# Kernel tuning notes

Measured on AMD Instinct MI355X. Metric: run time of the kernel, lower is better.

## Reference

```python
import jax, jax.numpy as jnp
import numpy as np

ATTN_HEADS = 4
NEG = -1e9
LN_EPS = 1e-5


def _ln(x, s, b):
    m = x.mean(-1, keepdims=True)
    v = ((x - m) ** 2).mean(-1, keepdims=True)
    return (x - m) * jax.lax.rsqrt(v + LN_EPS) * s + b


def setup_inputs() -> dict:
    key = jax.random.key(0)
    ks = jax.random.split(key, 40)
    B, L, D, FF, NL = 512, 192, 256, 1024, 2
    V, U, I = 30000, 100000, 50000
    Lp, Ln, NF = 30, 300, 13
    Lu = jax.random.randint(ks[0], (B,), 1, L // 2)
    Li = jax.random.randint(ks[1], (B,), 1, L // 2)
    inp = {
        'attr': jax.random.randint(ks[2], (B, L), 0, V),
        'attr_inds': jax.random.randint(ks[3], (B, L), 0, 3),
        'attr_tf': jax.random.uniform(ks[4], (B, L), dtype=jnp.float32),
        'attr_feat': jax.random.normal(ks[5], (B, L, NF), dtype=jnp.float32),
        'attr_lens': Lu + Li,
        'attr_lens_user': Lu,
        'attr_lens_item': Li,
        'user_ids': jax.random.randint(ks[6], (B,), 0, U),
        'item_ids': jax.random.randint(ks[7], (B,), 0, I),
        'pos_targets': jax.random.randint(ks[8], (B, Lp), 0, V),
        'pos_lens': jax.random.randint(ks[9], (B,), 1, Lp + 1),
        'neg_targets': jax.random.randint(ks[10], (B, Ln), 0, V),
        'neg_lens': jax.random.randint(ks[11], (B,), 1, Ln + 1),
        # embedding tables (uniform(-0.1,0.1) per f_init_weight)
        'attr_emb': jax.random.uniform(ks[12], (V, D), minval=-0.1, maxval=0.1),
        'ind_emb': jax.random.uniform(ks[13], (3, D), minval=-0.1, maxval=0.1),
        'user_emb_table': jax.random.uniform(ks[14], (U, D), minval=-0.1, maxval=0.1),
        'item_emb_table': jax.random.uniform(ks[15], (I, D), minval=-0.1, maxval=0.1),
        'out_emb_user': jax.random.uniform(ks[16], (V, 2 * D), minval=-0.1, maxval=0.1),
        'out_emb_item': jax.random.uniform(ks[17], (V, 2 * D), minval=-0.1, maxval=0.1),
        # attr-weight head: Linear(13,1) + sigmoid
        'feat_w': jax.random.normal(ks[18], (NF,)) * 0.02,
        'feat_b': jnp.zeros(()),
        # transformer encoder params, stacked over NL layers
        'Wqkv': jax.random.normal(ks[19], (NL, 3 * D, D)) * 0.02,
        'bqkv': jnp.zeros((NL, 3 * D)),
        'Wo': jax.random.normal(ks[20], (NL, D, D)) * 0.02,
        'bo': jnp.zeros((NL, D)),
        'ln1_s': jnp.ones((NL, D)), 'ln1_b': jnp.zeros((NL, D)),
        'W1': jax.random.normal(ks[21], (NL, FF, D)) * 0.02,
        'b1': jnp.zeros((NL, FF)),
        'W2': jax.random.normal(ks[22], (NL, D, FF)) * 0.02,
        'b2': jnp.zeros((NL, D)),
        'ln2_s': jnp.ones((NL, D)), 'ln2_b': jnp.zeros((NL, D)),
    }
    return inp


def reference(attr, attr_inds, attr_tf, attr_feat, attr_lens, attr_lens_user,
              attr_lens_item, user_ids, item_ids, pos_targets, pos_lens,
              neg_targets, neg_lens, attr_emb, ind_emb, user_emb_table,
              item_emb_table, out_emb_user, out_emb_item, feat_w, feat_b,
              Wqkv, bqkv, Wo, bo, ln1_s, ln1_b, W1, b1, W2, b2, ln2_s, ln2_b):
    B, L = attr.shape
    D = attr_emb.shape[1]
    NL = Wqkv.shape[0]
    Dh = D // ATTN_HEADS
    pos = jnp.arange(L)
    valid = pos[None, :] < attr_lens[:, None]  # [B,L] True = valid key

    x = attr_emb[attr] + ind_emb[attr_inds]  # [B,L,D]
    for l in range(NL):  # post-LN TransformerEncoderLayer, relu, no dropout
        qkv = x @ Wqkv[l].T + bqkv[l]
        q, k, v = jnp.split(qkv, 3, axis=-1)
        q = q.reshape(B, L, ATTN_HEADS, Dh).transpose(0, 2, 1, 3)
        k = k.reshape(B, L, ATTN_HEADS, Dh).transpose(0, 2, 1, 3)
        v = v.reshape(B, L, ATTN_HEADS, Dh).transpose(0, 2, 1, 3)
        scores = jnp.einsum('bhqd,bhkd->bhqk', q, k) / np.sqrt(Dh).astype(x.dtype)
        scores = jnp.where(valid[:, None, None, :], scores, NEG)
        a = jax.nn.softmax(scores, axis=-1)
        ctx = jnp.einsum('bhqk,bhkd->bhqd', a, v).transpose(0, 2, 1, 3).reshape(B, L, D)
        x = _ln(x + ctx @ Wo[l].T + bo[l], ln1_s[l], ln1_b[l])
        ff = jax.nn.relu(x @ W1[l].T + b1[l]) @ W2[l].T + b2[l]
        x = _ln(x + ff, ln2_s[l], ln2_b[l])

    # ragged weighted segment average over user span [0,Lu) and item span [Lu,Lu+Li)
    w_user = jax.nn.sigmoid(attr_feat @ feat_w + feat_b)  # [B,L]
    wted = x * attr_tf[..., None]
    umask = pos[None, :] < attr_lens_user[:, None]
    imask = (~umask) & (pos[None, :] < (attr_lens_user + attr_lens_item)[:, None])
    user_x = (wted * w_user[..., None] * umask[..., None]).sum(1) / attr_lens_user[:, None].astype(x.dtype)
    item_x = (wted * (1.0 - w_user)[..., None] * imask[..., None]).sum(1) / attr_lens_item[:, None].astype(x.dtype)

    user_out = jnp.concatenate([user_x, user_emb_table[user_ids]], axis=-1)  # [B,2D]
    item_out = jnp.concatenate([item_x, item_emb_table[item_ids]], axis=-1)

    def logit(t):
        return (jnp.einsum('bkd,bd->bk', out_emb_user[t], user_out)
                + jnp.einsum('bkd,bd->bk', out_emb_item[t], item_out))

    pos_logits = logit(pos_targets)
    neg_logits = logit(neg_targets)
    pmask = jnp.arange(pos_targets.shape[1])[None, :] < pos_lens[:, None]
    nmask = jnp.arange(neg_targets.shape[1])[None, :] < neg_lens[:, None]
    logits = jnp.concatenate([pos_logits, neg_logits], axis=-1)
    mask = jnp.concatenate([pmask, nmask], axis=-1)
    new_targets = jnp.concatenate([jnp.ones_like(pos_targets), jnp.zeros_like(neg_targets)], axis=1) * mask
    return logits, mask, new_targets
```

## Files before the change

kernel.cpp:

```cpp
#include <hip/hip_runtime.h>
#include <hip/hip_bf16.h>
#include <cstdint>
#include <cstddef>

#define B_ 512
#define L_ 192
#define D_ 256
#define H_ 4
#define DH_ 64
#define FF_ 1024
#define NL_ 2
#define LP_ 30
#define LNEG_ 300
#define NF_ 13
#define M_ (B_*L_)
#define NT_ 330
#define V_ 30000

typedef __attribute__((ext_vector_type(8))) short bf16x8;
typedef __attribute__((ext_vector_type(4))) float f32x4;

__device__ __forceinline__ ushort f2b(float f) {
  union { float f; uint32_t u; } v; v.f = f;
  uint32_t u = v.u;
  return (ushort)((u + 0x7FFFu + ((u >> 16) & 1u)) >> 16);
}
__device__ __forceinline__ float b2f(ushort u) {
  union { uint32_t u; float f; } v; v.u = (uint32_t)u << 16; return v.f;
}
__device__ __forceinline__ void stage16(const ushort* src, char* dst) {
  __builtin_amdgcn_global_load_lds((const __attribute__((address_space(1))) unsigned int*)src,
                                   (__attribute__((address_space(3))) unsigned int*)dst, 16, 0, 0);
}

__global__ __launch_bounds__(512) void k_prefix(
    const int* __restrict__ lens, int* __restrict__ off,
    int* __restrict__ ccnt, int* __restrict__ ccntp, int Bc, int nchunks)
{
  const int t = threadIdx.x;
  int s = 0;
  for (int i = 0; i < t; ++i) s += lens[i];
  off[t] = s;
  if (t == 511) off[512] = s + lens[511];
  if (t < nchunks) {
    int s2 = 0;
    const int c0 = t * Bc;
    for (int i = 0; i < Bc; ++i) s2 += lens[c0 + i];
    ccnt[t]  = s2;
    ccntp[t] = (s2 + 127) & ~127;
  }
}

__global__ __launch_bounds__(256) void k_f2b(const float* __restrict__ in, ushort* __restrict__ out) {
  const int i = (blockIdx.x*256 + threadIdx.x)*8;
  float4 a = *(const float4*)(in+i);
  float4 b = *(const float4*)(in+i+4);
  ushort4 o1; o1.x=f2b(a.x); o1.y=f2b(a.y); o1.z=f2b(a.z); o1.w=f2b(a.w);
  ushort4 o2; o2.x=f2b(b.x); o2.y=f2b(b.y); o2.z=f2b(b.z); o2.w=f2b(b.w);
  *(ushort4*)(out+i)   = o1;
  *(ushort4*)(out+i+4) = o2;
}

__global__ __launch_bounds__(256) void k_f2b4(
    const float* __restrict__ wq, const float* __restrict__ wo,
    const float* __restrict__ w1, const float* __restrict__ w2,
    ushort* __restrict__ oq, ushort* __restrict__ oo,
    ushort* __restrict__ o1, ushort* __restrict__ o2)
{
  int bb = blockIdx.x;
  const float* in; ushort* out; int base;
  if (bb < 192)      { in = wq; out = oq; base = bb; }
  else if (bb < 256) { in = wo; out = oo; base = bb - 192; }
  else if (bb < 512) { in = w1; out = o1; base = bb - 256; }
  else               { in = w2; out = o2; base = bb - 512; }
  const int i = base*2048 + threadIdx.x*8;
  float4 a = *(const float4*)(in+i);
  float4 b = *(const float4*)(in+i+4);
  ushort4 q1; q1.x=f2b(a.x); q1.y=f2b(a.y); q1.z=f2b(a.z); q1.w=f2b(a.w);
  ushort4 q2; q2.x=f2b(b.x); q2.y=f2b(b.y); q2.z=f2b(b.z); q2.w=f2b(b.w);
  *(ushort4*)(out+i)   = q1;
  *(ushort4*)(out+i+4) = q2;
}

__global__ __launch_bounds__(256) void k_embed(
    const int* __restrict__ attr, const int* __restrict__ inds,
    const int* __restrict__ lens, const int* __restrict__ off,
    const float* __restrict__ attr_emb, const float* __restrict__ ind_emb,
    ushort* __restrict__ xb)
{
  int idx = blockIdx.x*256 + threadIdx.x;
  int token = idx >> 6;
  int c = (idx & 63) * 4;
  int b = token / L_;
  int l = token - b*L_;
  if (l >= lens[b]) return;
  size_t crow = (size_t)off[b] + l;
  int a = attr[token];
  int id = inds[token];
  const float4 e  = *(const float4*)(attr_emb + (size_t)a*D_ + c);
  const float4 ie = *(const float4*)(ind_emb  + (size_t)id*D_ + c);
  ushort4 ob; ob.x=f2b(e.x+ie.x); ob.y=f2b(e.y+ie.y); ob.z=f2b(e.z+ie.z); ob.w=f2b(e.w+ie.w);
  *(ushort4*)(xb + crow*D_ + c) = ob;
}

template<int OUT_BF16, int RELU>
__global__ __launch_bounds__(256) void k_gemm_mfma(
    const ushort* __restrict__ A, const int* __restrict__ aoffp,
    const int* __restrict__ cntp,
    const ushort* __restrict__ W, const float* __restrict__ bias,
    void* __restrict__ Cv, int N, int K)
{
  if ((int)blockIdx.y * 128 >= *cntp) return;
  __shared__ alignas(16) ushort As[8192];
  __shared__ alignas(16) ushort Bs[8192];
  const int abase = *aoffp;
  const int tid = threadIdx.x;
  const int w = tid >> 6, l = tid & 63;
  const int g = l >> 4, c16 = l & 15;
  const int m0 = blockIdx.y*128, n0 = blockIdx.x*128;
  const int wr = w >> 1, wc = w & 1;
  const int swzr = (c16 & 7) << 4;

  f32x4 acc[4][4];
  #pragma unroll
  for (int i=0;i<4;++i)
    #pragma unroll
    for (int j=0;j<4;++j) acc[i][j] = (f32x4){0.f,0.f,0.f,0.f};

  for (int k0=0; k0<K; k0+=64) {
    #pragma unroll
    for (int i=0;i<4;++i) {
      const int li  = i*4096 + tid*16;
      const int row = li >> 7;
      const int col = ((li & 127) ^ ((row & 7) << 4)) >> 1;
      stage16(A + (size_t)(abase+m0+row)*K + k0 + col, (char*)(As) + i*4096 + w*1024);
      stage16(W + (size_t)(n0+row)*K + k0 + col,       (char*)(Bs) + i*4096 + w*1024);
    }
    __syncthreads();
    #pragma unroll
    for (int ks=0; ks<2; ++ks) {
      const int cb = ((g*16 + ks*64) ^ swzr) >> 1;
      bf16x8 af[4], bfr[4];
      #pragma unroll
      for (int i2=0;i2<4;++i2) {
        af[i2]  = *(const bf16x8*)(As + (size_t)(wr*64 + i2*16 + c16)*64 + cb);
        bfr[i2] = *(const bf16x8*)(Bs + (size_t)(wc*64 + i2*16 + c16)*64 + cb);
      }
      #pragma unroll
      for (int mi=0;mi<4;++mi)
        #pragma unroll
        for (int ni=0;ni<4;++ni)
          acc[mi][ni] = __builtin_amdgcn_mfma_f32_16x16x32_bf16(bfr[ni], af[mi], acc[mi][ni], 0,0,0);
    }
    __syncthreads();
  }
  #pragma unroll
  for (int ni=0;ni<4;++ni) {
    const int nc = n0 + wc*64 + ni*16 + 4*g;
    const float4 bv = *(const float4*)(bias + nc);
    #pragma unroll
    for (int mi=0;mi<4;++mi) {
      float v0 = acc[mi][ni][0] + bv.x;
      float v1 = acc[mi][ni][1] + bv.y;
      float v2 = acc[mi][ni][2] + bv.z;
      float v3 = acc[mi][ni][3] + bv.w;
      if (RELU) { v0=fmaxf(v0,0.f); v1=fmaxf(v1,0.f); v2=fmaxf(v2,0.f); v3=fmaxf(v3,0.f); }
      const size_t idx = (size_t)(m0 + wr*64 + mi*16 + c16)*N + nc;
      if (OUT_BF16) {
        ushort4 o; o.x=f2b(v0); o.y=f2b(v1); o.z=f2b(v2); o.w=f2b(v3);
        *(ushort4*)((ushort*)Cv + idx) = o;
      } else {
        float4 o; o.x=v0; o.y=v1; o.z=v2; o.w=v3;
        *(float4*)((float*)Cv + idx) = o;
      }
    }
  }
}

__global__ __launch_bounds__(512) void k_gemm_ln(
    const ushort* __restrict__ A,
    const int* __restrict__ cntp, const int* __restrict__ cnt,
    const int* __restrict__ xoffp,
    const ushort* __restrict__ W,
    const float* __restrict__ bias,
    const float* __restrict__ lns, const float* __restrict__ lnb,
    ushort* __restrict__ xb, int K)
{
  const int m0 = blockIdx.x*128;
  if (m0 >= *cntp) return;
  __shared__ alignas(16) ushort As[8192];
  __shared__ alignas(16) ushort Bs[16384];
  __shared__ float red[4][2][128];
  const int tid = threadIdx.x;
  const int w = tid >> 6, l = tid & 63;
  const int g = l >> 4, c16 = l & 15;
  const int wr = w >> 2, wc = w & 3;
  const int swzr = (c16 & 7) << 4;

  f32x4 acc[4][4];
  #pragma unroll
  for (int i=0;i<4;++i)
    #pragma unroll
    for (int j=0;j<4;++j) acc[i][j] = (f32x4){0.f,0.f,0.f,0.f};

  for (int k0=0; k0<K; k0+=64) {
    #pragma unroll
    for (int i=0;i<2;++i) {
      const int li  = i*8192 + tid*16;
      const int row = li >> 7;
      const int col = ((li & 127) ^ ((row & 7) << 4)) >> 1;
      stage16(A + (size_t)(m0+row)*K + k0 + col, (char*)(As) + i*8192 + w*1024);
    }
    #pragma unroll
    for (int i=0;i<4;++i) {
      const int li  = i*8192 + tid*16;
      const int row = li >> 7;
      const int col = ((li & 127) ^ ((row & 7) << 4)) >> 1;
      stage16(W + (size_t)row*K + k0 + col, (char*)(Bs) + i*8192 + w*1024);
    }
    __syncthreads();
    #pragma unroll
    for (int ks=0; ks<2; ++ks) {
      const int cb = ((g*16 + ks*64) ^ swzr) >> 1;
      bf16x8 af[4], bfr[4];
      #pragma unroll
      for (int i2=0;i2<4;++i2) {
        af[i2]  = *(const bf16x8*)(As + (size_t)(wr*64 + i2*16 + c16)*64 + cb);
        bfr[i2] = *(const bf16x8*)(Bs + (size_t)(wc*64 + i2*16 + c16)*64 + cb);
      }
      #pragma unroll
      for (int mi=0;mi<4;++mi)
        #pragma unroll
        for (int ni=0;ni<4;++ni)
          acc[mi][ni] = __builtin_amdgcn_mfma_f32_16x16x32_bf16(bfr[ni], af[mi], acc[mi][ni], 0,0,0);
    }
    __syncthreads();
  }

  const int xbase = *xoffp + m0;
  float4 bv[4], sv[4], bb[4];
  #pragma unroll
  for (int ni=0;ni<4;++ni) {
    const int nc = wc*64 + ni*16 + 4*g;
    bv[ni] = *(const float4*)(bias + nc);
    sv[ni] = *(const float4*)(lns + nc);
    bb[ni] = *(const float4*)(lnb + nc);
  }
  float ps[4], pq[4];
  #pragma unroll
  for (int mi=0;mi<4;++mi) {
    ps[mi]=0.f; pq[mi]=0.f;
    const int lrow = wr*64 + mi*16 + c16;
    const ushort* xr = xb + (size_t)(xbase + lrow)*256;
    #pragma unroll
    for (int ni=0;ni<4;++ni) {
      const int nc = wc*64 + ni*16 + 4*g;
      ushort4 rx = *(const ushort4*)(xr + nc);
      float y0 = acc[mi][ni][0] + bv[ni].x + b2f(rx.x);
      float y1 = acc[mi][ni][1] + bv[ni].y + b2f(rx.y);
      float y2 = acc[mi][ni][2] + bv[ni].z + b2f(rx.z);
      float y3 = acc[mi][ni][3] + bv[ni].w + b2f(rx.w);
      acc[mi][ni][0]=y0; acc[mi][ni][1]=y1; acc[mi][ni][2]=y2; acc[mi][ni][3]=y3;
      ps[mi] += (y0+y1)+(y2+y3);
      pq[mi] += (y0*y0+y1*y1)+(y2*y2+y3*y3);
    }
  }
  #pragma unroll
  for (int mi=0;mi<4;++mi) {
    ps[mi] += __shfl_xor(ps[mi], 16, 64);
    pq[mi] += __shfl_xor(pq[mi], 16, 64);
    ps[mi] += __shfl_xor(ps[mi], 32, 64);
    pq[mi] += __shfl_xor(pq[mi], 32, 64);
  }
  if (g == 0) {
    #pragma unroll
    for (int mi=0;mi<4;++mi) {
      const int lrow = wr*64 + mi*16 + c16;
      red[wc][0][lrow] = ps[mi];
      red[wc][1][lrow] = pq[mi];
    }
  }
  __syncthreads();
  const int cexact = *cnt;
  #pragma unroll
  for (int mi=0;mi<4;++mi) {
    const int lrow = wr*64 + mi*16 + c16;
    float tsum = red[0][0][lrow] + red[1][0][lrow] + red[2][0][lrow] + red[3][0][lrow];
    float tsq  = red[0][1][lrow] + red[1][1][lrow] + red[2][1][lrow] + red[3][1][lrow];
    float mean = tsum * (1.f/256.f);
    float var  = tsq * (1.f/256.f) - mean*mean;
    float inv  = rsqrtf(var + 1e-5f);
    if (m0 + lrow < cexact) {
      ushort* xbr = xb + (size_t)(xbase + lrow)*256;
      #pragma unroll
      for (int ni=0;ni<4;++ni) {
        const int nc = wc*64 + ni*16 + 4*g;
        ushort4 o;
        o.x = f2b((acc[mi][ni][0]-mean)*inv*sv[ni].x + bb[ni].x);
        o.y = f2b((acc[mi][ni][1]-mean)*inv*sv[ni].y + bb[ni].y);
        o.z = f2b((acc[mi][ni][2]-mean)*inv*sv[ni].z + bb[ni].z);
        o.w = f2b((acc[mi][ni][3]-mean)*inv*sv[ni].w + bb[ni].w);
        *(ushort4*)(xbr + nc) = o;
      }
    }
  }
}

__global__ __launch_bounds__(512) void k_ffn(
    const int* __restrict__ cntp, const int* __restrict__ cnt,
    const int* __restrict__ xoffp,
    const ushort* __restrict__ W1, const float* __restrict__ b1,
    const ushort* __restrict__ W2, const float* __restrict__ b2,
    const float* __restrict__ lns, const float* __restrict__ lnb,
    ushort* __restrict__ xb)
{
  const int m0 = blockIdx.x*64;
  if (m0 >= *cntp) return;
  __shared__ alignas(16) char lds[98304];
  char* Xs = lds;
  char* Wb = lds + 32768;
  char* Hs = lds + 81920;
  float* red = (float*)(lds + 32768);
  const int tid = threadIdx.x;
  const int w = tid >> 6, l = tid & 63;
  const int g = l >> 4, c16 = l & 15;
  const int wr = w >> 2, wc = w & 3;
  const int swzr = (c16 & 7) << 4;
  const int xbase = *xoffp + m0;

  int tokl[2];
  #pragma unroll
  for (int mi=0;mi<2;++mi) tokl[mi] = wr*32 + mi*16 + c16;

  auto stage_chunk = [&](int s, int q, char* dst) {
    #pragma unroll
    for (int i=0;i<2;++i) {
      const int li = i*8192 + tid*16;
      const int row = li >> 7;
      const int colb = (li & 127) ^ ((row & 7) << 4);
      const ushort* src;
      if (q < 4) src = W1 + (size_t)(s*128+row)*256 + q*64 + (colb>>1);
      else {
        const int t2 = q - 4;
        src = W2 + (size_t)((t2>>1)*128+row)*1024 + s*128 + (t2&1)*64 + (colb>>1);
      }
      stage16(src, dst + i*8192 + w*1024);
    }
  };

  #pragma unroll
  for (int i=0;i<4;++i) {
    const int li = i*8192 + tid*16;
    const int row = li >> 9;
    const int colb = (li & 511) ^ ((row & 7) << 4);
    stage16(xb + (size_t)(xbase+row)*256 + (colb>>1), Xs + i*8192 + w*1024);
  }
  stage_chunk(0, 0, Wb);
  stage_chunk(0, 1, Wb + 16384);
  asm volatile("s_waitcnt vmcnt(2) lgkmcnt(0)" ::: "memory");
  __builtin_amdgcn_s_barrier();
  __builtin_amdgcn_sched_barrier(0);

  f32x4 tac[2][4];
  #pragma unroll
  for (int i=0;i<2;++i)
    #pragma unroll
    for (int j=0;j<4;++j) tac[i][j] = (f32x4){0.f,0.f,0.f,0.f};

  int cur = 0;
  for (int s=0; s<8; ++s) {
    f32x4 hac[2][2];
    #pragma unroll
    for (int i=0;i<2;++i)
      #pragma unroll
      for (int j=0;j<2;++j) hac[i][j] = (f32x4){0.f,0.f,0.f,0.f};

    #pragma unroll
    for (int q=0; q<8; ++q) {
      if (q < 6) {
        stage_chunk(s, q+2, Wb + ((cur+2)%3)*16384);
      } else if (s < 7) {
        stage_chunk(s+1, q-6, Wb + ((cur+2)%3)*16384);
      }
      char* curbuf = Wb + cur*16384;

      if (q < 4) {
        #pragma unroll
        for (int ks=0; ks<2; ++ks) {
          const int cbw = (ks*64 + g*16) ^ swzr;
          bf16x8 w1f[2], xf[2];
          #pragma unroll
          for (int ni=0;ni<2;++ni)
            w1f[ni] = *(const bf16x8*)(curbuf + (wc*32 + ni*16 + c16)*128 + cbw);
          #pragma unroll
          for (int mi=0;mi<2;++mi)
            xf[mi] = *(const bf16x8*)(Xs + tokl[mi]*512 + ((q*128 + ks*64 + g*16) ^ swzr));
          #pragma unroll
          for (int mi=0;mi<2;++mi)
            #pragma unroll
            for (int ni=0;ni<2;++ni)
              hac[mi][ni] = __builtin_amdgcn_mfma_f32_16x16x32_bf16(w1f[ni], xf[mi], hac[mi][ni], 0,0,0);
        }
        if (q == 3) {
          #pragma unroll
          for (int ni=0;ni<2;++ni) {
            const int ffc = wc*32 + ni*16 + 4*g;
            const float4 bb1 = *(const float4*)(b1 + s*128 + ffc);
            #pragma unroll
            for (int mi=0;mi<2;++mi) {
              ushort4 o;
              o.x = f2b(fmaxf(hac[mi][ni][0] + bb1.x, 0.f));
              o.y = f2b(fmaxf(hac[mi][ni][1] + bb1.y, 0.f));
              o.z = f2b(fmaxf(hac[mi][ni][2] + bb1.z, 0.f));
              o.w = f2b(fmaxf(hac[mi][ni][3] + bb1.w, 0.f));
              *(ushort4*)(Hs + tokl[mi]*256 + ((ffc*2) ^ swzr)) = o;
            }
          }
        }
      } else {
        const int dh = (q-4) >> 1, kc2 = (q-4) & 1;
        #pragma unroll
        for (int ks=0; ks<2; ++ks) {
          const int cbw = (ks*64 + g*16) ^ swzr;
          bf16x8 w2f[2], hf[2];
          #pragma unroll
          for (int ni=0;ni<2;++ni)
            w2f[ni] = *(const bf16x8*)(curbuf + (wc*32 + ni*16 + c16)*128 + cbw);
          #pragma unroll
          for (int mi=0;mi<2;++mi)
            hf[mi] = *(const bf16x8*)(Hs + tokl[mi]*256 + ((kc2*128 + ks*64 + g*16) ^ swzr));
          #pragma unroll
          for (int mi=0;mi<2;++mi)
            #pragma unroll
            for (int ni=0;ni<2;++ni)
              tac[mi][dh*2+ni] = __builtin_amdgcn_mfma_f32_16x16x32_bf16(w2f[ni], hf[mi], tac[mi][dh*2+ni], 0,0,0);
        }
      }

      if (q >= 6) {
        if (s == 7) { asm volatile("s_waitcnt vmcnt(0) lgkmcnt(0)" ::: "memory"); }
        else        { asm volatile("s_waitcnt vmcnt(2) lgkmcnt(0)" ::: "memory"); }
      } else {
        asm volatile("s_waitcnt vmcnt(2) lgkmcnt(0)" ::: "memory");
      }
      __builtin_amdgcn_s_barrier();
      __builtin_amdgcn_sched_barrier(0);
      cur = (cur + 1) % 3;
    }
  }

  float4 bv[4], sv[4], bb[4];
  #pragma unroll
  for (int n=0;n<4;++n) {
    const int nc = (n>>1)*128 + wc*32 + (n&1)*16 + 4*g;
    bv[n] = *(const float4*)(b2 + nc);
    sv[n] = *(const float4*)(lns + nc);
    bb[n] = *(const float4*)(lnb + nc);
  }
  float ps[2], pq[2];
  #pragma unroll
  for (int mi=0;mi<2;++mi) {
    ps[mi]=0.f; pq[mi]=0.f;
    const ushort* xr = xb + (size_t)(xbase + tokl[mi])*256;
    #pragma unroll
    for (int n=0;n<4;++n) {
      const int nc = (n>>1)*128 + wc*32 + (n&1)*16 + 4*g;
      ushort4 rx = *(const ushort4*)(xr + nc);
      float y0 = tac[mi][n][0] + bv[n].x + b2f(rx.x);
      float y1 = tac[mi][n][1] + bv[n].y + b2f(rx.y);
      float y2 = tac[mi][n][2] + bv[n].z + b2f(rx.z);
      float y3 = tac[mi][n][3] + bv[n].w + b2f(rx.w);
      tac[mi][n][0]=y0; tac[mi][n][1]=y1; tac[mi][n][2]=y2; tac[mi][n][3]=y3;
      ps[mi] += (y0+y1)+(y2+y3);
      pq[mi] += (y0*y0+y1*y1)+(y2*y2+y3*y3);
    }
  }
  #pragma unroll
  for (int mi=0;mi<2;++mi) {
    ps[mi] += __shfl_xor(ps[mi], 16, 64);
    pq[mi] += __shfl_xor(pq[mi], 16, 64);
    ps[mi] += __shfl_xor(ps[mi], 32, 64);
    pq[mi] += __shfl_xor(pq[mi], 32, 64);
  }
  if (g == 0) {
    #pragma unroll
    for (int mi=0;mi<2;++mi) {
      red[(wc*2+0)*64 + tokl[mi]] = ps[mi];
      red[(wc*2+1)*64 + tokl[mi]] = pq[mi];
    }
  }
  __syncthreads();
  const int cexact = *cnt;
  #pragma unroll
  for (int mi=0;mi<2;++mi) {
    const int lrow = tokl[mi];
    float tsum = red[0*64+lrow] + red[2*64+lrow] + red[4*64+lrow] + red[6*64+lrow];
    float tsq  = red[1*64+lrow] + red[3*64+lrow] + red[5*64+lrow] + red[7*64+lrow];
    float mean = tsum * (1.f/256.f);
    float var  = tsq * (1.f/256.f) - mean*mean;
    float inv  = rsqrtf(var + 1e-5f);
    if (m0 + lrow < cexact) {
      ushort* xbr = xb + (size_t)(xbase + lrow)*256;
      #pragma unroll
      for (int n=0;n<4;++n) {
        const int nc = (n>>1)*128 + wc*32 + (n&1)*16 + 4*g;
        ushort4 o;
        o.x = f2b((tac[mi][n][0]-mean)*inv*sv[n].x + bb[n].x);
        o.y = f2b((tac[mi][n][1]-mean)*inv*sv[n].y + bb[n].y);
        o.z = f2b((tac[mi][n][2]-mean)*inv*sv[n].z + bb[n].z);
        o.w = f2b((tac[mi][n][3]-mean)*inv*sv[n].w + bb[n].w);
        *(ushort4*)(xbr + nc) = o;
      }
    }
  }
}

__global__ __launch_bounds__(256) void k_attn_mfma(
    const ushort* __restrict__ qkv, ushort* __restrict__ ctx,
    const int* __restrict__ offc)
{
  __shared__ alignas(16) char lds[81920];
  char* Kb = lds;
  char* Vt = lds + 24576;
  const int tid = threadIdx.x;
  const int w = tid >> 6, l = tid & 63;
  const int g = l >> 4, c = l & 15;
  char* Pw = lds + 57344 + w*6144;
  const int bl = blockIdx.x >> 2, h = blockIdx.x & 3;
  const int rowbase = offc[bl] - offc[0];
  const int len = offc[bl+1] - offc[bl];
  const int nkt = (len + 15) >> 4;
  const int nkf = (len + 31) >> 5;
  const ushort* base = qkv + (size_t)rowbase*768;
  ushort* cbase = ctx + (size_t)rowbase*256;

  const int lenk8 = nkt*16*8;
  for (int idx = tid; idx < lenk8; idx += 256) {
    int row = idx >> 3, ch = idx & 7;
    uint4 v = *(const uint4*)(base + (size_t)row*768 + 256 + h*64 + ch*8);
    *(uint4*)(Kb + ((row*128 + ch*16) ^ ((row&7)<<4))) = v;
  }
  {
    const int lenv = nkf*32;
    int d0 = (tid & 15)*4;
    for (int key = tid >> 4; key < lenv; key += 16) {
      ushort4 v = *(const ushort4*)(base + (size_t)key*768 + 512 + h*64 + d0);
      ushort vv[4] = {v.x, v.y, v.z, v.w};
      #pragma unroll
      for (int j=0;j<4;++j) {
        int d = d0 + j;
        *(ushort*)(Vt + ((d*512 + key*2) ^ ((d&7)<<4))) = vv[j];
      }
    }
  }
  __syncthreads();

  for (int t = nkt; t < 2*nkf; ++t) {
    #pragma unroll
    for (int r=0;r<4;++r) {
      int q = 4*g + r;
      *(ushort*)(Pw + (((t>>1)*1024 + q*64 + ((t&1)*16 + c)*2) ^ (((q>>2)&3)<<4))) = 0;
    }
  }

  const int nst = (len + 15) >> 4;
  for (int s = w; s < nst; s += 4) {
    const ushort* qp = base + (size_t)(s*16 + c)*768 + h*64 + g*8;
    bf16x8 aq0 = *(const bf16x8*)qp;
    bf16x8 aq1 = *(const bf16x8*)(qp + 32);

    f32x4 sc[12];
    #pragma unroll
    for (int t=0;t<12;++t) {
      sc[t] = (f32x4){0.f,0.f,0.f,0.f};
      if (t < nkt) {
        int ba0 = ((t*16 + c)*128 + g*16)      ^ ((c&7)<<4);
        int ba1 = ((t*16 + c)*128 + g*16 + 64) ^ ((c&7)<<4);
        bf16x8 k0 = *(const bf16x8*)(Kb + ba0);
        bf16x8 k1 = *(const bf16x8*)(Kb + ba1);
        sc[t] = __builtin_amdgcn_mfma_f32_16x16x32_bf16(aq0, k0, sc[t], 0,0,0);
        sc[t] = __builtin_amdgcn_mfma_f32_16x16x32_bf16(aq1, k1, sc[t], 0,0,0);
        if (t == nkt-1 && t*16 + c >= len)
          sc[t] = (f32x4){-1e30f,-1e30f,-1e30f,-1e30f};
      }
    }
    float mr[4] = {-1e30f,-1e30f,-1e30f,-1e30f};
    #pragma unroll
    for (int t=0;t<12;++t) if (t<nkt) {
      #pragma unroll
      for (int r=0;r<4;++r) mr[r] = fmaxf(mr[r], sc[t][r]);
    }
    #pragma unroll
    for (int r=0;r<4;++r) {
      mr[r] = fmaxf(mr[r], __shfl_xor(mr[r], 1, 16));
      mr[r] = fmaxf(mr[r], __shfl_xor(mr[r], 2, 16));
      mr[r] = fmaxf(mr[r], __shfl_xor(mr[r], 4, 16));
      mr[r] = fmaxf(mr[r], __shfl_xor(mr[r], 8, 16));
    }
    float sr[4] = {0.f,0.f,0.f,0.f};
    #pragma unroll
    for (int t=0;t<12;++t) if (t<nkt) {
      #pragma unroll
      for (int r=0;r<4;++r) {
        float p = __expf((sc[t][r] - mr[r]) * 0.125f);
        sr[r] += p;
        int q = 4*g + r;
        *(ushort*)(Pw + (((t>>1)*1024 + q*64 + ((t&1)*16 + c)*2) ^ (((q>>2)&3)<<4))) = f2b(p);
      }
    }
    #pragma unroll
    for (int r=0;r<4;++r) {
      sr[r] += __shfl_xor(sr[r], 1, 16);
      sr[r] += __shfl_xor(sr[r], 2, 16);
      sr[r] += __shfl_xor(sr[r], 4, 16);
      sr[r] += __shfl_xor(sr[r], 8, 16);
    }
    f32x4 oa[4];
    #pragma unroll
    for (int dt=0;dt<4;++dt) oa[dt] = (f32x4){0.f,0.f,0.f,0.f};
    #pragma unroll
    for (int kf=0;kf<6;++kf) if (kf<nkf) {
      bf16x8 pf = *(const bf16x8*)(Pw + ((kf*1024 + c*64 + g*16) ^ (((c>>2)&3)<<4)));
      #pragma unroll
      for (int dt=0;dt<4;++dt) {
        int d = dt*16 + c;
        bf16x8 vf = *(const bf16x8*)(Vt + ((d*512 + kf*64 + g*16) ^ ((d&7)<<4)));
        oa[dt] = __builtin_amdgcn_mfma_f32_16x16x32_bf16(pf, vf, oa[dt], 0,0,0);
      }
    }
    float inv[4];
    #pragma unroll
    for (int r=0;r<4;++r) inv[r] = 1.f / sr[r];
    ushort* orow = cbase + (size_t)(s*16)*256 + h*64;
    #pragma unroll
    for (int r=0;r<4;++r) {
      int q = 4*g + r;
      if (s*16 + q < len) {
        #pragma unroll
        for (int dt=0;dt<4;++dt)
          orow[(size_t)q*256 + dt*16 + c] = f2b(oa[dt][r] * inv[r]);
      }
    }
  }
}

__global__ __launch_bounds__(256) void k_pool(
    const ushort* __restrict__ xb, const int* __restrict__ off,
    const float* __restrict__ attr_tf, const float* __restrict__ attr_feat,
    const int* __restrict__ lens_u, const int* __restrict__ lens_i,
    const int* __restrict__ user_ids, const int* __restrict__ item_ids,
    const float* __restrict__ user_tab, const float* __restrict__ item_tab,
    const float* __restrict__ feat_w, const float* __restrict__ feat_b,
    float* __restrict__ user_out, float* __restrict__ item_out)
{
  __shared__ float wu[L_], tf[L_];
  const int b = blockIdx.x;
  const int t = threadIdx.x;
  if (t < L_) {
    const float* f = attr_feat + ((size_t)b*L_ + t)*NF_;
    float sacc = feat_b[0];
    #pragma unroll
    for (int j=0;j<NF_;++j) sacc = fmaf(f[j], feat_w[j], sacc);
    wu[t] = 1.f/(1.f+__expf(-sacc));
    tf[t] = attr_tf[b*L_+t];
  }
  __syncthreads();
  const int Lu = lens_u[b], Li = lens_i[b];
  const ushort* xrow = xb + (size_t)off[b]*D_;
  float su=0.f, si=0.f;
  for (int l=0;l<Lu+Li;++l) {
    float val = b2f(xrow[(size_t)l*D_ + t]) * tf[l];
    if (l < Lu) su = fmaf(val, wu[l], su);
    else        si = fmaf(val, 1.f-wu[l], si);
  }
  user_out[(size_t)b*512 + t]       = su/(float)Lu;
  item_out[(size_t)b*512 + t]       = si/(float)Li;
  user_out[(size_t)b*512 + 256 + t] = user_tab[(size_t)user_ids[b]*D_ + t];
  item_out[(size_t)b*512 + 256 + t] = item_tab[(size_t)item_ids[b]*D_ + t];
}

__global__ __launch_bounds__(256) void k_logits(
    const int* __restrict__ pos_t, const int* __restrict__ neg_t,
    const int* __restrict__ pos_l, const int* __restrict__ neg_l,
    const ushort* __restrict__ oeu, const ushort* __restrict__ oei,
    const float* __restrict__ user_out, const float* __restrict__ item_out,
    float* __restrict__ out)
{
  const int g = blockIdx.x*4 + (threadIdx.x >> 6);
  const int lane = threadIdx.x & 63;
  const int b = g / NT_;
  const int k = g - b*NT_;
  const int tid_ = (k < LP_) ? pos_t[b*LP_ + k] : neg_t[b*LNEG_ + (k-LP_)];
  const ushort* eu = oeu + (size_t)tid_*512;
  const ushort* ei = oei + (size_t)tid_*512;
  const float* uo = user_out + (size_t)b*512;
  const float* io = item_out + (size_t)b*512;
  const int d0 = lane*8;
  float s = 0.f;
  ushort4 a0 = *(const ushort4*)(eu+d0), a1 = *(const ushort4*)(eu+d0+4);
  float4 u0 = *(const float4*)(uo+d0), u1 = *(const float4*)(uo+d0+4);
  s += b2f(a0.x)*u0.x + b2f(a0.y)*u0.y + b2f(a0.z)*u0.z + b2f(a0.w)*u0.w;
  s += b2f(a1.x)*u1.x + b2f(a1.y)*u1.y + b2f(a1.z)*u1.z + b2f(a1.w)*u1.w;
  ushort4 c0 = *(const ushort4*)(ei+d0), c1 = *(const ushort4*)(ei+d0+4);
  float4 i0 = *(const float4*)(io+d0), i1 = *(const float4*)(io+d0+4);
  s += b2f(c0.x)*i0.x + b2f(c0.y)*i0.y + b2f(c0.z)*i0.z + b2f(c0.w)*i0.w;
  s += b2f(c1.x)*i1.x + b2f(c1.y)*i1.y + b2f(c1.z)*i1.z + b2f(c1.w)*i1.w;
  #pragma unroll
  for (int off=32; off>0; off>>=1) s += __shfl_xor(s, off, 64);
  if (lane == 0) {
    out[(size_t)b*NT_ + k] = s;
    float mv, nt;
    if (k < LP_) { mv = (k < pos_l[b]) ? 1.f : 0.f; nt = mv; }
    else         { mv = ((k - LP_) < neg_l[b]) ? 1.f : 0.f; nt = 0.f; }
    out[(size_t)B_*NT_   + (size_t)b*NT_ + k] = mv;
    out[(size_t)2*B_*NT_ + (size_t)b*NT_ + k] = nt;
  }
}

extern "C" void kernel_launch(void* const* d_in, const int* in_sizes, int n_in,
                              void* d_out, int out_size, void* d_ws, size_t ws_size,
                              hipStream_t stream)
{
  const int*   attr      = (const int*)d_in[0];
  const int*   attr_inds = (const int*)d_in[1];
  const float* attr_tf   = (const float*)d_in[2];
  const float* attr_feat = (const float*)d_in[3];
  const int*   attr_lens = (const int*)d_in[4];
  const int*   lens_u    = (const int*)d_in[5];
  const int*   lens_i    = (const int*)d_in[6];
  const int*   user_ids  = (const int*)d_in[7];
  const int*   item_ids  = (const int*)d_in[8];
  const int*   pos_t     = (const int*)d_in[9];
  const int*   pos_l     = (const int*)d_in[10];
  const int*   neg_t     = (const int*)d_in[11];
  const int*   neg_l     = (const int*)d_in[12];
  const float* attr_emb  = (const float*)d_in[13];
  const float* ind_emb   = (const float*)d_in[14];
  const float* user_tab  = (const float*)d_in[15];
  const float* item_tab  = (const float*)d_in[16];
  const float* oeu       = (const float*)d_in[17];
  const float* oei       = (const float*)d_in[18];
  const float* feat_w    = (const float*)d_in[19];
  const float* feat_b    = (const float*)d_in[20];
  const float* Wqkv      = (const float*)d_in[21];
  const float* bqkv      = (const float*)d_in[22];
  const float* Wo        = (const float*)d_in[23];
  const float* bo        = (const float*)d_in[24];
  const float* ln1s      = (const float*)d_in[25];
  const float* ln1b      = (const float*)d_in[26];
  const float* W1        = (const float*)d_in[27];
  const float* b1        = (const float*)d_in[28];
  const float* W2        = (const float*)d_in[29];
  const float* b2        = (const float*)d_in[30];
  const float* ln2s      = (const float*)d_in[31];
  const float* ln2b      = (const float*)d_in[32];

  int* ioff  = (int*)d_ws;
  int* ccnt  = ioff + 520;
  int* ccntp = ccnt + 64;
  float* ws = (float*)d_ws + 768;
  float* uo = ws;
  float* io = uo + (size_t)B_*512;
  ushort* xb   = (ushort*)(io + (size_t)B_*512);
  ushort* wq_b = xb + (size_t)M_*D_;
  ushort* wo_b = wq_b + (size_t)2*768*256;
  ushort* w1_b = wo_b + (size_t)2*256*256;
  ushort* w2_b = w1_b + (size_t)2*1024*256;
  ushort* oeu_b = w2_b + (size_t)2*256*1024;
  ushort* oei_b = oeu_b + (size_t)V_*512;
  float* scratch = (float*)(oei_b + (size_t)V_*512);

  const size_t fixed_floats = 768 + (size_t)B_*1024 + (size_t)M_*(D_/2) + 786432 + (size_t)V_*512;
  int Bc = 8;
  for (int cand = 512; cand >= 8; cand >>= 1) {
    size_t need = (fixed_floats + (size_t)cand*L_*512) * sizeof(float);
    if (need <= ws_size) { Bc = cand; break; }
  }
  const int nchunks = B_ / Bc;
  const size_t Mc = (size_t)Bc * L_;

  float* out = (float*)d_out;

  k_prefix<<<1, 512, 0, stream>>>(attr_lens, ioff, ccnt, ccntp, Bc, nchunks);
  k_f2b4<<<768, 256, 0, stream>>>(Wqkv, Wo, W1, W2, wq_b, wo_b, w1_b, w2_b);
  k_f2b<<<(V_*512)/2048, 256, 0, stream>>>(oeu, oeu_b);
  k_f2b<<<(V_*512)/2048, 256, 0, stream>>>(oei, oei_b);
  k_embed<<<M_*64/256, 256, 0, stream>>>(attr, attr_inds, attr_lens, ioff, attr_emb, ind_emb, xb);

  for (int l=0; l<NL_; ++l) {
    const float* bqkv_l = bqkv + (size_t)l*768;
    const float* bo_l   = bo   + (size_t)l*D_;
    const float* b1_l   = b1   + (size_t)l*FF_;
    const float* b2_l   = b2   + (size_t)l*D_;
    for (int c=0; c<nchunks; ++c) {
      const int* offc = ioff + c*Bc;
      const int* cntp = ccntp + c;
      const int* cnt  = ccnt + c;
      ushort* qkv_b = (ushort*)scratch;
      ushort* ctx_b = (ushort*)(scratch + Mc*384);

      k_gemm_mfma<1,0><<<dim3(768/128, Mc/128), 256, 0, stream>>>(
          xb, offc, cntp, wq_b + (size_t)l*768*256, bqkv_l, qkv_b, 768, 256);
      k_attn_mfma<<<Bc*H_, 256, 0, stream>>>(qkv_b, ctx_b, offc);
      k_gemm_ln<<<Mc/128, 512, 0, stream>>>(
          ctx_b, cntp, cnt, offc, wo_b + (size_t)l*256*256, bo_l,
          ln1s + (size_t)l*D_, ln1b + (size_t)l*D_, xb, 256);
      k_ffn<<<Mc/64, 512, 0, stream>>>(
          cntp, cnt, offc, w1_b + (size_t)l*1024*256, b1_l,
          w2_b + (size_t)l*256*1024, b2_l,
          ln2s + (size_t)l*D_, ln2b + (size_t)l*D_, xb);
    }
  }
  k_pool<<<B_, 256, 0, stream>>>(xb, ioff, attr_tf, attr_feat, lens_u, lens_i, user_ids, item_ids,
                                 user_tab, item_tab, feat_w, feat_b, uo, io);
  k_logits<<<B_*NT_/4, 256, 0, stream>>>(pos_t, neg_t, pos_l, neg_l, oeu_b, oei_b, uo, io, out);
}
```

Before: 640.3 us.

## Hold FFN input tile in registers and double-buffer weights to cut LDS

Loads each wave's slice of the 64-token input tile into registers once, so the FFN kernel no longer keeps a 32KB X buffer in LDS. The weight ring drops from triple to double buffering, bringing LDS from 96KB to 48KB and allowing more blocks per CU. The hand-tuned waitcnt/barrier sequence becomes plain __syncthreads, which waits for all outstanding loads each step and shortens prefetch distance. It also adds 16 bf16x8 registers per thread, which risks spills or lower register occupancy at 512 threads.

```diff
diff --git a/kernel.cpp b/kernel.cpp
--- a/kernel.cpp
+++ b/kernel.cpp
@@ -316,11 +316,10 @@
 {
   const int m0 = blockIdx.x*64;
   if (m0 >= *cntp) return;
-  __shared__ alignas(16) char lds[98304];
-  char* Xs = lds;
-  char* Wb = lds + 32768;
-  char* Hs = lds + 81920;
-  float* red = (float*)(lds + 32768);
+  __shared__ alignas(16) char lds[49152];
+  char* Wb = lds;
+  char* Hs = lds + 32768;
+  float* red = (float*)lds;
   const int tid = threadIdx.x;
   const int w = tid >> 6, l = tid & 63;
   const int g = l >> 4, c16 = l & 15;
@@ -353,13 +352,18 @@
     const int li = i*8192 + tid*16;
     const int row = li >> 9;
     const int colb = (li & 511) ^ ((row & 7) << 4);
-    stage16(xb + (size_t)(xbase+row)*256 + (colb>>1), Xs + i*8192 + w*1024);
-  }
+    stage16(xb + (size_t)(xbase+row)*256 + (colb>>1), lds + i*8192 + w*1024);
+  }
+  __syncthreads();
+  bf16x8 xreg[2][8];
+  #pragma unroll
+  for (int mi=0;mi<2;++mi)
+    #pragma unroll
+    for (int f=0;f<8;++f)
+      xreg[mi][f] = *(const bf16x8*)(lds + tokl[mi]*512 + ((f*64 + g*16) ^ swzr));
+  __syncthreads();
   stage_chunk(0, 0, Wb);
-  stage_chunk(0, 1, Wb + 16384);
-  asm volatile("s_waitcnt vmcnt(2) lgkmcnt(0)" ::: "memory");
-  __builtin_amdgcn_s_barrier();
-  __builtin_amdgcn_sched_barrier(0);
+  __syncthreads();
 
   f32x4 tac[2][4];
   #pragma unroll
@@ -367,7 +371,7 @@
     #pragma unroll
     for (int j=0;j<4;++j) tac[i][j] = (f32x4){0.f,0.f,0.f,0.f};
 
-  int cur = 0;
+  int pp = 0;
   for (int s=0; s<8; ++s) {
     f32x4 hac[2][2];
     #pragma unroll
@@ -377,29 +381,23 @@
 
     #pragma unroll
     for (int q=0; q<8; ++q) {
-      if (q < 6) {
-        stage_chunk(s, q+2, Wb + ((cur+2)%3)*16384);
-      } else if (s < 7) {
-        stage_chunk(s+1, q-6, Wb + ((cur+2)%3)*16384);
-      }
-      char* curbuf = Wb + cur*16384;
+      if (q < 7)      stage_chunk(s, q+1, Wb + (pp^1)*16384);
+      else if (s < 7) stage_chunk(s+1, 0, Wb + (pp^1)*16384);
+      char* curbuf = Wb + pp*16384;
 
       if (q < 4) {
         #pragma unroll
         for (int ks=0; ks<2; ++ks) {
           const int cbw = (ks*64 + g*16) ^ swzr;
-          bf16x8 w1f[2], xf[2];
+          bf16x8 w1f[2];
           #pragma unroll
           for (int ni=0;ni<2;++ni)
             w1f[ni] = *(const bf16x8*)(curbuf + (wc*32 + ni*16 + c16)*128 + cbw);
           #pragma unroll
           for (int mi=0;mi<2;++mi)
-            xf[mi] = *(const bf16x8*)(Xs + tokl[mi]*512 + ((q*128 + ks*64 + g*16) ^ swzr));
-          #pragma unroll
-          for (int mi=0;mi<2;++mi)
             #pragma unroll
             for (int ni=0;ni<2;++ni)
-              hac[mi][ni] = __builtin_amdgcn_mfma_f32_16x16x32_bf16(w1f[ni], xf[mi], hac[mi][ni], 0,0,0);
+              hac[mi][ni] = __builtin_amdgcn_mfma_f32_16x16x32_bf16(w1f[ni], xreg[mi][q*2+ks], hac[mi][ni], 0,0,0);
         }
         if (q == 3) {
           #pragma unroll
@@ -436,16 +434,8 @@
               tac[mi][dh*2+ni] = __builtin_amdgcn_mfma_f32_16x16x32_bf16(w2f[ni], hf[mi], tac[mi][dh*2+ni], 0,0,0);
         }
       }
-
-      if (q >= 6) {
-        if (s == 7) { asm volatile("s_waitcnt vmcnt(0) lgkmcnt(0)" ::: "memory"); }
-        else        { asm volatile("s_waitcnt vmcnt(2) lgkmcnt(0)" ::: "memory"); }
-      } else {
-        asm volatile("s_waitcnt vmcnt(2) lgkmcnt(0)" ::: "memory");
-      }
-      __builtin_amdgcn_s_barrier();
-      __builtin_amdgcn_sched_barrier(0);
-      cur = (cur + 1) % 3;
+      __syncthreads();
+      pp ^= 1;
     }
   }
 
```

After: 661.8 us. 1.03x slower.
